# Kernel optimization log

Measured on AMD Instinct MI355X. Metric: run time of the kernel, lower is better.

## Reference

```python
import jax, jax.numpy as jnp
import numpy as np

N = 131072        # total points
M = 34            # max_num_neighbors (hard-coded in forward)
K = 15            # kernel points (torch-points3d default for 3D KPConv)
C_IN, C_OUT = 32, 64
POINT_INFLUENCE = 0.04        # prev_grid_size * sigma
KERNEL_RADIUS = 1.5 * POINT_INFLUENCE  # _INFLUENCE_TO_RADIUS * point_influence
BN_EPS = 1e-5
NEG_SLOPE = 0.2


def setup_inputs() -> dict:
    key = jax.random.key(0)
    ks = jax.random.split(key, 6)
    # points in a [0, 0.1]^3 box so random neighbors can fall inside the influence radius
    xyz = jax.random.uniform(ks[0], (N, 3), jnp.float32) * 0.1
    feats = jax.random.normal(ks[1], (N, C_IN), jnp.float32)
    neighbor_idx = jax.random.randint(ks[2], (N, M), 0, N, dtype=jnp.int32)
    # fixed kernel-point disposition: points inside a sphere of radius KERNEL_RADIUS
    kp_dir = jax.random.normal(ks[3], (K, 3), jnp.float32)
    kp_dir = kp_dir / jnp.linalg.norm(kp_dir, axis=1, keepdims=True)
    kp_rad = jax.random.uniform(ks[4], (K, 1), jnp.float32) ** (1.0 / 3.0)
    k_points = kp_dir * kp_rad * KERNEL_RADIUS
    weight = jax.random.normal(ks[5], (K, C_IN, C_OUT), jnp.float32) / np.sqrt(K * C_IN)
    gamma = jnp.ones((C_OUT,), jnp.float32)
    beta = jnp.zeros((C_OUT,), jnp.float32)
    return {"xyz": xyz, "feats": feats, "neighbor_idx": neighbor_idx,
            "weight": weight, "k_points": k_points, "gamma": gamma, "beta": beta}


def _kpconv(xyz, feats, neighbor_idx, weight, k_points):
    # shadow point / shadow feature row for out-of-range neighbor index == N
    sup = jnp.concatenate([xyz, jnp.full((1, 3), 1e6, xyz.dtype)], axis=0)
    f = jnp.concatenate([feats, jnp.zeros((1, feats.shape[1]), feats.dtype)], axis=0)
    # [N, M, 3] neighbor offsets relative to each query point
    nb = sup[neighbor_idx] - xyz[:, None, :]
    # [N, M, K] distance from each neighbor to each kernel point
    diff = nb[:, :, None, :] - k_points[None, None, :, :]
    dist = jnp.sqrt(jnp.sum(diff * diff, axis=-1))
    # linear kernel influence, 'sum' aggregation
    w = jnp.maximum(0.0, 1.0 - dist / POINT_INFLUENCE)          # [N, M, K]
    nb_f = f[neighbor_idx]                                       # [N, M, C_IN]
    wf = jnp.einsum('nmk,nmc->nkc', w, nb_f)                     # [N, K, C_IN]
    return jnp.einsum('nkc,kcd->nd', wf, weight)                 # [N, C_OUT]


def reference(xyz, feats, neighbor_idx, weight, k_points, gamma, beta):
    out = _kpconv(xyz, feats, neighbor_idx, weight, k_points)
    # FastBatchNorm1d (training-mode batch statistics) + LeakyReLU(0.2)
    mean = jnp.mean(out, axis=0)
    var = jnp.mean((out - mean) ** 2, axis=0)
    out = (out - mean) * jax.lax.rsqrt(var + BN_EPS) * gamma + beta
    return jnp.where(out >= 0, out, NEG_SLOPE * out)
```

## Files before the change

### kernel.cpp

```cpp
#include <hip/hip_runtime.h>

#define NPTS 131072
#define MNBR 34
#define KP 15
#define CIN 32
#define COUT 64
#define INV_INFL 25.0f
#define BN_EPS 1e-5f
#define NEG_SLOPE 0.2f
#define PPB 16
#define NBLK (NPTS / PPB)
#define NSB 512
#define SKIP_D2 0.01f

typedef unsigned short u16;
typedef unsigned int u32;
typedef short short8 __attribute__((ext_vector_type(8)));
typedef float f32x4 __attribute__((ext_vector_type(4)));

static __device__ __forceinline__ u16 f2bf(float f) {
    u32 x = __float_as_uint(f);
    x += 0x7fffu + ((x >> 16) & 1u);
    return (u16)(x >> 16);
}
static __device__ __forceinline__ u32 pk2bf(float lo, float hi) {
    u32 a = __float_as_uint(lo) + 0x8000u;
    u32 b = __float_as_uint(hi) + 0x8000u;
    return (a >> 16) | (b & 0xffff0000u);
}
static __device__ __forceinline__ float rdlanef(float v, int l) {
    return __uint_as_float(__builtin_amdgcn_readlane(__float_as_uint(v), l));
}

#define WS_WT   0u
#define WS_SCSH 65536u
#define WS_PART 131072u
#define WS_XY   393216u
#define WS_FB   2490624u

__global__ __launch_bounds__(256) void prep(const float* __restrict__ Wg,
                                            const float* __restrict__ feats,
                                            const float* __restrict__ xyz,
                                            u16* __restrict__ WT, float4* __restrict__ XY,
                                            uint2* __restrict__ FB2) {
    int b = blockIdx.x;
    if (b < 120) {
        int i2 = b * 256 + threadIdx.x;
        WT[(i2 & 63) * 480 + (i2 >> 6)] = f2bf(Wg[i2]);
    } else if (b < 633) {
        int r = (b - 120) * 256 + threadIdx.x;
        if (r <= NPTS) {
            float4 v;
            if (r < NPTS) v = make_float4(xyz[3 * r], xyz[3 * r + 1], xyz[3 * r + 2], 0.f);
            else          v = make_float4(1e6f, 1e6f, 1e6f, 0.f);
            XY[r] = v;
        }
    } else {
        int g2 = (b - 633) * 256 + threadIdx.x;
        if (g2 < 1048584) {
            uint2 v = make_uint2(0u, 0u);
            if (g2 < 1048576) {
                float4 f = ((const float4*)feats)[g2];
                v.x = (u32)f2bf(f.x) | ((u32)f2bf(f.y) << 16);
                v.y = (u32)f2bf(f.z) | ((u32)f2bf(f.w) << 16);
            }
            FB2[g2] = v;
        }
    }
}

__global__ __launch_bounds__(128, 3) void kpconv_conv(
    const float* __restrict__ xyz, const int* __restrict__ nbr,
    const float4* __restrict__ XY, const u32* __restrict__ FBu,
    const u16* __restrict__ WT, const float* __restrict__ kpts,
    float* __restrict__ out)
{
    __shared__ u32 wf[PPB * 256];
    __shared__ float4 offs4[2][2][64];

    const int tid = threadIdx.x, lane = tid & 63, wave = tid >> 6;
    const int q = lane >> 4, t = lane & 15;
    const int pbase = blockIdx.x * PPB + wave * 8;

    float axt = 0.f, ayt = 0.f, azt = 0.f, ckt = 1e30f;
    if (t < KP) {
        float kx = kpts[3 * t], ky = kpts[3 * t + 1], kz = kpts[3 * t + 2];
        axt = -2.f * kx; ayt = -2.f * ky; azt = -2.f * kz;
        ckt = fmaf(kx, kx, fmaf(ky, ky, kz * kz));
    }
    const int wslot = (lane & ~7) | ((lane ^ (lane >> 3)) & 7);
    const int sl = q * 8;

    auto ldnbr = [&](int pp) {
        int v = NPTS;
        if (lane < MNBR) v = nbr[(size_t)(pbase + pp) * MNBR + lane];
        if ((u32)v > (u32)NPTS) v = NPTS;
        return v;
    };

    float qxv[8], qyv[8], qzv[8];
    #pragma unroll
    for (int p = 0; p < 8; ++p) {
        const int n1 = pbase + p;
        qxv[p] = xyz[3 * n1]; qyv[p] = xyz[3 * n1 + 1]; qzv[p] = xyz[3 * n1 + 2];
    }

    u32 fbA[8] = {0,0,0,0,0,0,0,0};
    u32 fbB[8] = {0,0,0,0,0,0,0,0};
    u32 fbC[8] = {0,0,0,0,0,0,0,0};
    u32 d32A = 0, d33A = 0, d32B = 0, d33B = 0, d32N = 0, d33N = 0;

    int ix0 = ldnbr(0);
    int ix1 = ldnbr(1);
    int ixF = ldnbr(2);
    int ix3 = ldnbr(3);
    float4 pn0 = XY[ix0];
    float4 pn1 = XY[ix1];
    float4 pnF = XY[ixF];

    {
        float ox = pn0.x - qxv[0], oy = pn0.y - qyv[0], oz = pn0.z - qzv[0];
        float ow = fmaf(ox, ox, fmaf(oy, oy, oz * oz));
        offs4[wave][0][wslot] = make_float4(ox, oy, oz, ow);
        #pragma unroll
        for (int j = 0; j < 8; ++j) {
            float dj = __shfl(ow, sl + j, 64);
            u32 r0 = (u32)__shfl(ix0, sl + j, 64);
            if (dj < SKIP_D2) fbA[j] = FBu[(size_t)r0 * 16 + t];
        }
        float w32 = rdlanef(ow, 32), w33 = rdlanef(ow, 33);
        int r32 = __builtin_amdgcn_readlane(ix0, 32);
        int r33 = __builtin_amdgcn_readlane(ix0, 33);
        if (w32 < SKIP_D2) d32A = FBu[(size_t)r32 * 16 + t];
        if (w33 < SKIP_D2) d33A = FBu[(size_t)r33 * 16 + t];
    }
    float o1x, o1y, o1z, o1w;
    {
        o1x = pn1.x - qxv[1]; o1y = pn1.y - qyv[1]; o1z = pn1.z - qzv[1];
        o1w = fmaf(o1x, o1x, fmaf(o1y, o1y, o1z * o1z));
        #pragma unroll
        for (int j = 0; j < 8; ++j) {
            float dj = __shfl(o1w, sl + j, 64);
            u32 r1 = (u32)__shfl(ix1, sl + j, 64);
            if (dj < SKIP_D2) fbB[j] = FBu[(size_t)r1 * 16 + t];
        }
        float w32 = rdlanef(o1w, 32), w33 = rdlanef(o1w, 33);
        int r32 = __builtin_amdgcn_readlane(ix1, 32);
        int r33 = __builtin_amdgcn_readlane(ix1, 33);
        if (w32 < SKIP_D2) d32B = FBu[(size_t)r32 * 16 + t];
        if (w33 < SKIP_D2) d33B = FBu[(size_t)r33 * 16 + t];
    }

    #pragma unroll
    for (int p = 0; p < 8; ++p) {
        int ixN = NPTS;
        if (p < 4) ixN = ldnbr(p + 4);
        float4 pnN = make_float4(1e6f, 1e6f, 1e6f, 0.f);
        if (p < 5) pnN = XY[ix3];
        float o2x = 0.f, o2y = 0.f, o2z = 0.f, o2w = 1e30f;
        if (p < 6) {
            o2x = pnF.x - qxv[p + 2]; o2y = pnF.y - qyv[p + 2]; o2z = pnF.z - qzv[p + 2];
            o2w = fmaf(o2x, o2x, fmaf(o2y, o2y, o2z * o2z));
            #pragma unroll
            for (int j = 0; j < 8; ++j) {
                float dj = __shfl(o2w, sl + j, 64);
                u32 r2 = (u32)__shfl(ixF, sl + j, 64);
                if (dj < SKIP_D2) fbC[j] = FBu[(size_t)r2 * 16 + t];
            }
            float w32 = rdlanef(o2w, 32), w33 = rdlanef(o2w, 33);
            int r32 = __builtin_amdgcn_readlane(ixF, 32);
            int r33 = __builtin_amdgcn_readlane(ixF, 33);
            if (w32 < SKIP_D2) d32N = FBu[(size_t)r32 * 16 + t];
            if (w33 < SKIP_D2) d33N = FBu[(size_t)r33 * 16 + t];
        }
        if (p < 7) {
            offs4[wave][(p + 1) & 1][wslot] = make_float4(o1x, o1y, o1z, o1w);
        }

        const float4* ob = &offs4[wave][p & 1][0];
        float wj[8];
        #pragma unroll
        for (int j = 0; j < 8; ++j) {
            float4 o = ob[q * 8 + (j ^ q)];
            float d2 = fmaf(o.x, axt, fmaf(o.y, ayt, fmaf(o.z, azt, ckt))) + o.w;
            float dd = __builtin_amdgcn_sqrtf(d2);
            wj[j] = fmaxf(0.f, fmaf(dd, -INV_INFL, 1.f));
        }
        union { short8 v; u32 d[4]; } a1, a2, e1, o1u, e2, o2u;
        #pragma unroll
        for (int i = 0; i < 4; ++i) a1.d[i] = pk2bf(wj[2 * i], wj[2 * i + 1]);
        {
            float4 oA = ob[36], oB = ob[37];
            float dA = __builtin_amdgcn_sqrtf(fmaf(oA.x, axt, fmaf(oA.y, ayt, fmaf(oA.z, azt, ckt))) + oA.w);
            float dB = __builtin_amdgcn_sqrtf(fmaf(oB.x, axt, fmaf(oB.y, ayt, fmaf(oB.z, azt, ckt))) + oB.w);
            float wA = fmaxf(0.f, fmaf(dA, -INV_INFL, 1.f));
            float wB = fmaxf(0.f, fmaf(dB, -INV_INFL, 1.f));
            a2.d[0] = (q == 0) ? pk2bf(wA, wB) : 0u;
            a2.d[1] = 0; a2.d[2] = 0; a2.d[3] = 0;
        }
        #pragma unroll
        for (int i = 0; i < 4; ++i) {
            u32 aa = fbA[2 * i], bb2 = fbA[2 * i + 1];
            e1.d[i] = (aa & 0xffffu) | (bb2 << 16);
            o1u.d[i] = (aa >> 16) | (bb2 & 0xffff0000u);
        }
        {
            u32 lo = (d32A & 0xffffu) | (d33A << 16);
            u32 hi = (d32A >> 16) | (d33A & 0xffff0000u);
            e2.d[0] = (q == 0) ? lo : 0u;  e2.d[1] = 0; e2.d[2] = 0; e2.d[3] = 0;
            o2u.d[0] = (q == 0) ? hi : 0u; o2u.d[1] = 0; o2u.d[2] = 0; o2u.d[3] = 0;
        }
        f32x4 c0 = {0.f, 0.f, 0.f, 0.f}, c1 = {0.f, 0.f, 0.f, 0.f};
        c0 = __builtin_amdgcn_mfma_f32_16x16x32_bf16(a1.v, e1.v, c0, 0, 0, 0);
        c0 = __builtin_amdgcn_mfma_f32_16x16x32_bf16(a2.v, e2.v, c0, 0, 0, 0);
        c1 = __builtin_amdgcn_mfma_f32_16x16x32_bf16(a1.v, o1u.v, c1, 0, 0, 0);
        c1 = __builtin_amdgcn_mfma_f32_16x16x32_bf16(a2.v, o2u.v, c1, 0, 0, 0);

        const int row = wave * 8 + p;
        #pragma unroll
        for (int r = 0; r < 4; ++r) {
            int ko = q * 4 + r;
            u32 pk = pk2bf(c0[r], c1[r]);
            int unit = ko * 4 + (t >> 2);
            wf[row * 256 + ((unit ^ (row & 7)) << 2) + (t & 3)] = pk;
        }

        #pragma unroll
        for (int j = 0; j < 8; ++j) { fbA[j] = fbB[j]; fbB[j] = fbC[j]; }
        d32A = d32B; d33A = d33B; d32B = d32N; d33B = d33N;
        pnF = pnN; o1x = o2x; o1y = o2y; o1z = o2z; o1w = o2w;
        ixF = ix3; ix3 = ixN;
    }
    __syncthreads();

    const int wcol0 = (wave * 2 + 0) * 16 + t;
    const int wcol1 = (wave * 2 + 1) * 16 + t;
    f32x4 A0 = {0.f, 0.f, 0.f, 0.f}, A1 = {0.f, 0.f, 0.f, 0.f};
    const u16* wt0 = WT + wcol0 * 480 + q * 8;
    const u16* wt1 = WT + wcol1 * 480 + q * 8;
    #pragma unroll
    for (int ks = 0; ks < KP; ++ks) {
        const int u = ks * 4 + q;
        short8 a   = *(const short8*)&wf[t * 256 + ((u ^ (t & 7)) << 2)];
        short8 bb0 = *(const short8*)(wt0 + ks * 32);
        short8 bb1 = *(const short8*)(wt1 + ks * 32);
        A0 = __builtin_amdgcn_mfma_f32_16x16x32_bf16(a, bb0, A0, 0, 0, 0);
        A1 = __builtin_amdgcn_mfma_f32_16x16x32_bf16(a, bb1, A1, 0, 0, 0);
    }
    const int base = blockIdx.x * PPB;
    #pragma unroll
    for (int r = 0; r < 4; ++r) {
        out[(base + q * 4 + r) * COUT + wcol0] = A0[r];
        out[(base + q * 4 + r) * COUT + wcol1] = A1[r];
    }
}

__global__ __launch_bounds__(256) void stat_partial(const float* __restrict__ out,
                                                    float* __restrict__ Part)
{
    const int tid = threadIdx.x, lane = tid & 63, wave = tid >> 6;
    const int u = tid & 15;
    const int pr = tid >> 4;
    const float4* O = (const float4*)out + (size_t)blockIdx.x * 4096;
    float s0 = 0.f, s1 = 0.f, s2 = 0.f, s3 = 0.f;
    float q0 = 0.f, q1 = 0.f, q2 = 0.f, q3 = 0.f;
    #pragma unroll
    for (int it = 0; it < 16; ++it) {
        float4 v = O[(it * 16 + pr) * 16 + u];
        s0 += v.x; q0 = fmaf(v.x, v.x, q0);
        s1 += v.y; q1 = fmaf(v.y, v.y, q1);
        s2 += v.z; q2 = fmaf(v.z, v.z, q2);
        s3 += v.w; q3 = fmaf(v.w, v.w, q3);
    }
    s0 += __shfl_xor(s0, 16, 64); s0 += __shfl_xor(s0, 32, 64);
    s1 += __shfl_xor(s1, 16, 64); s1 += __shfl_xor(s1, 32, 64);
    s2 += __shfl_xor(s2, 16, 64); s2 += __shfl_xor(s2, 32, 64);
    s3 += __shfl_xor(s3, 16, 64); s3 += __shfl_xor(s3, 32, 64);
    q0 += __shfl_xor(q0, 16, 64); q0 += __shfl_xor(q0, 32, 64);
    q1 += __shfl_xor(q1, 16, 64); q1 += __shfl_xor(q1, 32, 64);
    q2 += __shfl_xor(q2, 16, 64); q2 += __shfl_xor(q2, 32, 64);
    q3 += __shfl_xor(q3, 16, 64); q3 += __shfl_xor(q3, 32, 64);
    __shared__ float red[4][16][8];
    if (lane < 16) {
        float* r = red[wave][lane];
        r[0] = s0; r[1] = s1; r[2] = s2; r[3] = s3;
        r[4] = q0; r[5] = q1; r[6] = q2; r[7] = q3;
    }
    __syncthreads();
    if (tid < 128) {
        int ch = tid >> 1, su = tid & 1;
        int uu = ch >> 2, c = ch & 3;
        float v = red[0][uu][su * 4 + c] + red[1][uu][su * 4 + c]
                + red[2][uu][su * 4 + c] + red[3][uu][su * 4 + c];
        Part[blockIdx.x * 128 + tid] = v;
    }
}

__global__ __launch_bounds__(256) void bn_reduce(
    const float* __restrict__ Part,
    const float* __restrict__ gamma, const float* __restrict__ beta,
    float* __restrict__ scsh)
{
    const int ch = blockIdx.x;
    const int tid = threadIdx.x;
    float s = 0.f, qq = 0.f;
    for (int b = tid; b < NSB; b += 256) {
        s  += Part[b * 128 + ch * 2];
        qq += Part[b * 128 + ch * 2 + 1];
    }
    #pragma unroll
    for (int off = 1; off < 64; off <<= 1) {
        s += __shfl_xor(s, off, 64); qq += __shfl_xor(qq, off, 64);
    }
    __shared__ float red[8];
    const int w = tid >> 6;
    if ((tid & 63) == 0) { red[w * 2] = s; red[w * 2 + 1] = qq; }
    __syncthreads();
    if (tid == 0) {
        s  = red[0] + red[2] + red[4] + red[6];
        qq = red[1] + red[3] + red[5] + red[7];
        float mean = s * (1.0f / NPTS);
        float var  = qq * (1.0f / NPTS) - mean * mean;
        float sc = gamma[ch] * rsqrtf(var + BN_EPS);
        scsh[ch] = sc;
        scsh[64 + ch] = beta[ch] - mean * sc;
    }
}

__global__ __launch_bounds__(256) void bn_apply(
    float* __restrict__ out, const float* __restrict__ scsh)
{
    __shared__ float sc[64], sh[64];
    const int tid = threadIdx.x;
    if (tid < 64) { sc[tid] = scsh[tid]; sh[tid] = scsh[64 + tid]; }
    __syncthreads();
    const int gid = blockIdx.x * 256 + tid;
    float4 v = ((const float4*)out)[gid];
    const int c0 = (gid * 4) & 63;
    float y0 = fmaf(v.x, sc[c0 + 0], sh[c0 + 0]);
    float y1 = fmaf(v.y, sc[c0 + 1], sh[c0 + 1]);
    float y2 = fmaf(v.z, sc[c0 + 2], sh[c0 + 2]);
    float y3 = fmaf(v.w, sc[c0 + 3], sh[c0 + 3]);
    float4 w;
    w.x = fmaxf(y0, NEG_SLOPE * y0);
    w.y = fmaxf(y1, NEG_SLOPE * y1);
    w.z = fmaxf(y2, NEG_SLOPE * y2);
    w.w = fmaxf(y3, NEG_SLOPE * y3);
    ((float4*)out)[gid] = w;
}

extern "C" void kernel_launch(void* const* d_in, const int* in_sizes, int n_in,
                              void* d_out, int out_size, void* d_ws, size_t ws_size,
                              hipStream_t stream) {
    (void)in_sizes; (void)n_in; (void)out_size; (void)ws_size;
    const float* xyz   = (const float*)d_in[0];
    const float* feats = (const float*)d_in[1];
    const int*   nbr   = (const int*)d_in[2];
    const float* Wg    = (const float*)d_in[3];
    const float* kpts  = (const float*)d_in[4];
    const float* gamma = (const float*)d_in[5];
    const float* beta  = (const float*)d_in[6];
    float* out = (float*)d_out;
    char* ws = (char*)d_ws;
    u16*    WT   = (u16*)(ws + WS_WT);
    float*  scsh = (float*)(ws + WS_SCSH);
    float*  Part = (float*)(ws + WS_PART);
    float4* XY   = (float4*)(ws + WS_XY);
    u32*    FBu  = (u32*)(ws + WS_FB);

    prep<<<dim3(4730), dim3(256), 0, stream>>>(Wg, feats, xyz, WT, XY, (uint2*)FBu);
    kpconv_conv<<<dim3(NBLK), dim3(128), 0, stream>>>(xyz, nbr, XY, FBu, WT, kpts, out);
    stat_partial<<<dim3(NSB), dim3(256), 0, stream>>>(out, Part);
    bn_reduce<<<dim3(64), dim3(256), 0, stream>>>(Part, gamma, beta, scsh);
    bn_apply<<<dim3((NPTS * COUT) / (256 * 4)), dim3(256), 0, stream>>>(out, scsh);
}
```

Baseline: 220.8 us.

## Compute kernel weights early and skip feature gathers with zero influence

Moves the kernel-point influence weight computation into the prefetch stage, two points ahead of use, and carries the packed bf16 weights through a three-deep register pipeline. Feature rows are now gathered only when a ballot shows at least one kernel point in the 16-lane group has nonzero influence, replacing the coarse squared-distance threshold. The offset shared buffer shrinks to a single slot per wave. This should cut gather traffic for neighbors outside every kernel point's influence and take the weight math off the MFMA critical path, at the cost of more live registers and extra ballots and shuffles per stage.

```diff
diff --git a/kernel.cpp b/kernel.cpp
--- a/kernel.cpp
+++ b/kernel.cpp
@@ -11,10 +11,10 @@
 #define PPB 16
 #define NBLK (NPTS / PPB)
 #define NSB 512
-#define SKIP_D2 0.01f
 
 typedef unsigned short u16;
 typedef unsigned int u32;
+typedef unsigned long long u64;
 typedef short short8 __attribute__((ext_vector_type(8)));
 typedef float f32x4 __attribute__((ext_vector_type(4)));
 
@@ -27,9 +27,6 @@
     u32 a = __float_as_uint(lo) + 0x8000u;
     u32 b = __float_as_uint(hi) + 0x8000u;
     return (a >> 16) | (b & 0xffff0000u);
-}
-static __device__ __forceinline__ float rdlanef(float v, int l) {
-    return __uint_as_float(__builtin_amdgcn_readlane(__float_as_uint(v), l));
 }
 
 #define WS_WT   0u
@@ -76,7 +73,7 @@
     float* __restrict__ out)
 {
     __shared__ u32 wf[PPB * 256];
-    __shared__ float4 offs4[2][2][64];
+    __shared__ float4 offs4[2][64];
 
     const int tid = threadIdx.x, lane = tid & 63, wave = tid >> 6;
     const int q = lane >> 4, t = lane & 15;
@@ -108,7 +105,47 @@
     u32 fbA[8] = {0,0,0,0,0,0,0,0};
     u32 fbB[8] = {0,0,0,0,0,0,0,0};
     u32 fbC[8] = {0,0,0,0,0,0,0,0};
-    u32 d32A = 0, d33A = 0, d32B = 0, d33B = 0, d32N = 0, d33N = 0;
+    u32 d32A = 0, d33A = 0, d32B = 0, d33B = 0, d32C = 0, d33C = 0;
+    u32 a1A[4], a1B[4], a1C[4];
+    u32 a2A = 0, a2B = 0, a2C = 0;
+
+    #define STAGE(P, ixP, pnP, a1X, a2X, fbX, d32X, d33X)                         \
+    {                                                                              \
+        float ox = (pnP).x - qxv[P], oy = (pnP).y - qyv[P], oz = (pnP).z - qzv[P]; \
+        float ow = fmaf(ox, ox, fmaf(oy, oy, oz * oz));                            \
+        offs4[wave][wslot] = make_float4(ox, oy, oz, ow);                          \
+        const float4* ob = &offs4[wave][0];                                        \
+        float wjs[8];                                                              \
+        _Pragma("unroll")                                                          \
+        for (int j = 0; j < 8; ++j) {                                              \
+            float4 o = ob[q * 8 + (j ^ q)];                 \
+            float d2 = fmaf(o.x, axt, fmaf(o.y, ayt, fmaf(o.z, azt, ckt))) + o.w;  \
+            float dd = __builtin_amdgcn_sqrtf(d2);                                 \
+            wjs[j] = fmaxf(0.f, fmaf(dd, -INV_INFL, 1.f));                         \
+        }                                                                          \
+        _Pragma("unroll")                                                          \
+        for (int i = 0; i < 4; ++i) a1X[i] = pk2bf(wjs[2 * i], wjs[2 * i + 1]);    \
+        float4 oA = ob[36], oB = ob[37];                   \
+        float dA = __builtin_amdgcn_sqrtf(fmaf(oA.x, axt, fmaf(oA.y, ayt, fmaf(oA.z, azt, ckt))) + oA.w); \
+        float dB = __builtin_amdgcn_sqrtf(fmaf(oB.x, axt, fmaf(oB.y, ayt, fmaf(oB.z, azt, ckt))) + oB.w); \
+        float wA = fmaxf(0.f, fmaf(dA, -INV_INFL, 1.f));                           \
+        float wB = fmaxf(0.f, fmaf(dB, -INV_INFL, 1.f));                           \
+        a2X = (q == 0) ? pk2bf(wA, wB) : 0u;                                       \
+        _Pragma("unroll")                                                          \
+        for (int j = 0; j < 8; ++j) {                                              \
+            u64 bj = __ballot(wjs[j] > 0.f);    \
+            u32 half = (q & 2) ? (u32)(bj >> 32) : (u32)bj;                        \
+            u32 m16 = (half >> ((q & 1) * 16)) & 0xffffu;                          \
+            u32 r = (u32)__shfl((ixP), sl + j, 64);                                \
+            if (m16) fbX[j] = FBu[(size_t)r * 16 + t];                             \
+        }                                                                          \
+        u64 b32 = __ballot(wA > 0.f);                                              \
+        u64 b33 = __ballot(wB > 0.f);                                              \
+        int r32 = __builtin_amdgcn_readlane((ixP), 32);                            \
+        int r33 = __builtin_amdgcn_readlane((ixP), 33);                            \
+        if (b32) d32X = FBu[(size_t)r32 * 16 + t];                                 \
+        if (b33) d33X = FBu[(size_t)r33 * 16 + t];                                 \
+    }
 
     int ix0 = ldnbr(0);
     int ix1 = ldnbr(1);
@@ -118,38 +155,8 @@
     float4 pn1 = XY[ix1];
     float4 pnF = XY[ixF];
 
-    {
-        float ox = pn0.x - qxv[0], oy = pn0.y - qyv[0], oz = pn0.z - qzv[0];
-        float ow = fmaf(ox, ox, fmaf(oy, oy, oz * oz));
-        offs4[wave][0][wslot] = make_float4(ox, oy, oz, ow);
-        #pragma unroll
-        for (int j = 0; j < 8; ++j) {
-            float dj = __shfl(ow, sl + j, 64);
-            u32 r0 = (u32)__shfl(ix0, sl + j, 64);
-            if (dj < SKIP_D2) fbA[j] = FBu[(size_t)r0 * 16 + t];
-        }
-        float w32 = rdlanef(ow, 32), w33 = rdlanef(ow, 33);
-        int r32 = __builtin_amdgcn_readlane(ix0, 32);
-        int r33 = __builtin_amdgcn_readlane(ix0, 33);
-        if (w32 < SKIP_D2) d32A = FBu[(size_t)r32 * 16 + t];
-        if (w33 < SKIP_D2) d33A = FBu[(size_t)r33 * 16 + t];
-    }
-    float o1x, o1y, o1z, o1w;
-    {
-        o1x = pn1.x - qxv[1]; o1y = pn1.y - qyv[1]; o1z = pn1.z - qzv[1];
-        o1w = fmaf(o1x, o1x, fmaf(o1y, o1y, o1z * o1z));
-        #pragma unroll
-        for (int j = 0; j < 8; ++j) {
-            float dj = __shfl(o1w, sl + j, 64);
-            u32 r1 = (u32)__shfl(ix1, sl + j, 64);
-            if (dj < SKIP_D2) fbB[j] = FBu[(size_t)r1 * 16 + t];
-        }
-        float w32 = rdlanef(o1w, 32), w33 = rdlanef(o1w, 33);
-        int r32 = __builtin_amdgcn_readlane(ix1, 32);
-        int r33 = __builtin_amdgcn_readlane(ix1, 33);
-        if (w32 < SKIP_D2) d32B = FBu[(size_t)r32 * 16 + t];
-        if (w33 < SKIP_D2) d33B = FBu[(size_t)r33 * 16 + t];
-    }
+    STAGE(0, ix0, pn0, a1A, a2A, fbA, d32A, d33A);
+    STAGE(1, ix1, pn1, a1B, a2B, fbB, d32B, d33B);
 
     #pragma unroll
     for (int p = 0; p < 8; ++p) {
@@ -157,47 +164,13 @@
         if (p < 4) ixN = ldnbr(p + 4);
         float4 pnN = make_float4(1e6f, 1e6f, 1e6f, 0.f);
         if (p < 5) pnN = XY[ix3];
-        float o2x = 0.f, o2y = 0.f, o2z = 0.f, o2w = 1e30f;
         if (p < 6) {
-            o2x = pnF.x - qxv[p + 2]; o2y = pnF.y - qyv[p + 2]; o2z = pnF.z - qzv[p + 2];
-            o2w = fmaf(o2x, o2x, fmaf(o2y, o2y, o2z * o2z));
-            #pragma unroll
-            for (int j = 0; j < 8; ++j) {
-                float dj = __shfl(o2w, sl + j, 64);
-                u32 r2 = (u32)__shfl(ixF, sl + j, 64);
-                if (dj < SKIP_D2) fbC[j] = FBu[(size_t)r2 * 16 + t];
-            }
-            float w32 = rdlanef(o2w, 32), w33 = rdlanef(o2w, 33);
-            int r32 = __builtin_amdgcn_readlane(ixF, 32);
-            int r33 = __builtin_amdgcn_readlane(ixF, 33);
-            if (w32 < SKIP_D2) d32N = FBu[(size_t)r32 * 16 + t];
-            if (w33 < SKIP_D2) d33N = FBu[(size_t)r33 * 16 + t];
-        }
-        if (p < 7) {
-            offs4[wave][(p + 1) & 1][wslot] = make_float4(o1x, o1y, o1z, o1w);
-        }
-
-        const float4* ob = &offs4[wave][p & 1][0];
-        float wj[8];
-        #pragma unroll
-        for (int j = 0; j < 8; ++j) {
-            float4 o = ob[q * 8 + (j ^ q)];
-            float d2 = fmaf(o.x, axt, fmaf(o.y, ayt, fmaf(o.z, azt, ckt))) + o.w;
-            float dd = __builtin_amdgcn_sqrtf(d2);
-            wj[j] = fmaxf(0.f, fmaf(dd, -INV_INFL, 1.f));
-        }
+            STAGE(p + 2, ixF, pnF, a1C, a2C, fbC, d32C, d33C);
+        }
+
         union { short8 v; u32 d[4]; } a1, a2, e1, o1u, e2, o2u;
-        #pragma unroll
-        for (int i = 0; i < 4; ++i) a1.d[i] = pk2bf(wj[2 * i], wj[2 * i + 1]);
-        {
-            float4 oA = ob[36], oB = ob[37];
-            float dA = __builtin_amdgcn_sqrtf(fmaf(oA.x, axt, fmaf(oA.y, ayt, fmaf(oA.z, azt, ckt))) + oA.w);
-            float dB = __builtin_amdgcn_sqrtf(fmaf(oB.x, axt, fmaf(oB.y, ayt, fmaf(oB.z, azt, ckt))) + oB.w);
-            float wA = fmaxf(0.f, fmaf(dA, -INV_INFL, 1.f));
-            float wB = fmaxf(0.f, fmaf(dB, -INV_INFL, 1.f));
-            a2.d[0] = (q == 0) ? pk2bf(wA, wB) : 0u;
-            a2.d[1] = 0; a2.d[2] = 0; a2.d[3] = 0;
-        }
+        a1.d[0] = a1A[0]; a1.d[1] = a1A[1]; a1.d[2] = a1A[2]; a1.d[3] = a1A[3];
+        a2.d[0] = a2A; a2.d[1] = 0; a2.d[2] = 0; a2.d[3] = 0;
         #pragma unroll
         for (int i = 0; i < 4; ++i) {
             u32 aa = fbA[2 * i], bb2 = fbA[2 * i + 1];
@@ -226,10 +199,12 @@
         }
 
         #pragma unroll
-        for (int j = 0; j < 8; ++j) { fbA[j] = fbB[j]; fbB[j] = fbC[j]; }
-        d32A = d32B; d33A = d33B; d32B = d32N; d33B = d33N;
-        pnF = pnN; o1x = o2x; o1y = o2y; o1z = o2z; o1w = o2w;
-        ixF = ix3; ix3 = ixN;
+        for (int j = 0; j < 8; ++j) { fbA[j] = fbB[j]; fbB[j] = fbC[j]; fbC[j] = 0; }
+        d32A = d32B; d33A = d33B; d32B = d32C; d33B = d33C; d32C = 0; d33C = 0;
+        #pragma unroll
+        for (int i = 0; i < 4; ++i) { a1A[i] = a1B[i]; a1B[i] = a1C[i]; }
+        a2A = a2B; a2B = a2C;
+        pnF = pnN; ixF = ix3; ix3 = ixN;
     }
     __syncthreads();
 
```

After: 216.7 us. About the same (-1.9%).
